# Kernel optimization log

Measured on AMD Instinct MI355X. Metric: run time of the kernel, lower is better.

The kernel has to match this reference:

```python
import jax, jax.numpy as jnp
import numpy as np

B, S, D_IN, D_OUT = 4, 2048, 1024, 1024

def setup_inputs() -> dict:
    key = jax.random.key(0)
    kx, kq, kk, kv = jax.random.split(key, 4)
    x = jax.random.normal(kx, (B, S, D_IN), dtype=jnp.float32)
    # nn.Linear weights are [d_out, d_in]; init scale ~ 1/sqrt(d_in)
    sc = 1.0 / np.sqrt(D_IN)
    Wq = jax.random.uniform(kq, (D_OUT, D_IN), minval=-sc, maxval=sc, dtype=jnp.float32)
    Wk = jax.random.uniform(kk, (D_OUT, D_IN), minval=-sc, maxval=sc, dtype=jnp.float32)
    Wv = jax.random.uniform(kv, (D_OUT, D_IN), minval=-sc, maxval=sc, dtype=jnp.float32)
    return {"x": x, "Wq": Wq, "Wk": Wk, "Wv": Wv}

def reference(x, Wq, Wk, Wv):
    # QKV projections (Linear without bias): y = x @ W.T
    q = jnp.einsum('bsd,od->bso', x, Wq)
    k = jnp.einsum('bsd,od->bso', x, Wk)
    v = jnp.einsum('bsd,od->bso', x, Wv)
    scores = jnp.einsum('bqo,bko->bqk', q, k)
    # NOTE: original code calls masked_fill non-in-place and discards the
    # result, so no causal mask is actually applied. Faithful: no mask.
    scale = 1.0 / jnp.sqrt(jnp.asarray(k.shape[-1], dtype=scores.dtype))
    weights = jax.nn.softmax(scores * scale, axis=-1)
    # dropout p=0.0 -> identity
    return jnp.einsum('bqk,bko->bqo', weights, v)
```

## Files before the change

### kernel.cpp

```cpp
#include <hip/hip_runtime.h>
#include <hip/hip_bf16.h>
#include <stdint.h>


typedef short bf16x8 __attribute__((ext_vector_type(8)));
typedef float f32x4  __attribute__((ext_vector_type(4)));
typedef unsigned short ushortx8 __attribute__((ext_vector_type(8)));

__device__ __forceinline__ unsigned short f2bf(float f) {
  unsigned u = __float_as_uint(f);
  u += 0x7fff + ((u >> 16) & 1);
  return (unsigned short)(u >> 16);
}

__global__ __launch_bounds__(256) void cvt_bf16(const float* __restrict__ src,
                                                unsigned short* __restrict__ dst) {
  int i = (blockIdx.x * 256 + threadIdx.x) * 4;
  float4 v = *(const float4*)(src + i);
  ushort4 o;
  o.x = f2bf(v.x); o.y = f2bf(v.y); o.z = f2bf(v.z); o.w = f2bf(v.w);
  *(ushort4*)(dst + i) = o;
}

__device__ __forceinline__ void gload_lds16(const void* g, void* l) {
  __builtin_amdgcn_global_load_lds(
      (const __attribute__((address_space(1))) unsigned int*)g,
      (__attribute__((address_space(3))) unsigned int*)l, 16, 0, 0);
}

template<int STORE>
__global__ __launch_bounds__(256, 2) void gemm_nt(
    const unsigned short* __restrict__ A, const unsigned short* __restrict__ B,
    void* __restrict__ Cv, int lda, int ldb, int ldc, int K,
    long strideA, long strideB, long strideC, float scale) {
  __shared__ __align__(16) unsigned short lds[2][2][128 * 32];
  const int tid  = threadIdx.x;
  const int lane = tid & 63;
  const int wid  = tid >> 6;
  const int bz   = blockIdx.z;
  const unsigned short* Ab = A + (size_t)bz * strideA;
  const unsigned short* Bb = B + (size_t)bz * strideB;
  const int row0 = blockIdx.x * 128;
  const int col0 = blockIdx.y * 128;

  f32x4 acc[4][4];
#pragma unroll
  for (int m = 0; m < 4; ++m)
#pragma unroll
    for (int n = 0; n < 4; ++n) acc[m][n] = f32x4{0.f, 0.f, 0.f, 0.f};

  const int KT = K >> 5;

  auto stage = [&](int buf, int kt) {
    const int k0 = kt << 5;
#pragma unroll
    for (int it = 0; it < 2; ++it) {
      int j   = it * 256 + tid;
      int r   = j >> 2;
      int kg  = j & 3;
      int kgS = kg ^ ((r >> 1) & 3);
      gload_lds16(Ab + (size_t)(row0 + r) * lda + k0 + kgS * 8, &lds[buf][0][j * 8]);
      gload_lds16(Bb + (size_t)(col0 + r) * ldb + k0 + kgS * 8, &lds[buf][1][j * 8]);
    }
  };

  stage(0, 0);
  int buf = 0;
  for (int kt = 0; kt < KT; ++kt) {
    __syncthreads();
    if (kt + 1 < KT) stage(buf ^ 1, kt + 1);
    const unsigned short* As = &lds[buf][0][0];
    const unsigned short* Bs = &lds[buf][1][0];
    const int kg = lane >> 4;
    const int lr = lane & 15;
    bf16x8 af[4], bfr[4];
#pragma unroll
    for (int m = 0; m < 4; ++m) {
      int r = ((wid >> 1) * 64) + m * 16 + lr;
      af[m] = *(const bf16x8*)(As + r * 32 + ((kg ^ ((r >> 1) & 3)) * 8));
    }
#pragma unroll
    for (int n = 0; n < 4; ++n) {
      int c = ((wid & 1) * 64) + n * 16 + lr;
      bfr[n] = *(const bf16x8*)(Bs + c * 32 + ((kg ^ ((c >> 1) & 3)) * 8));
    }
#pragma unroll
    for (int m = 0; m < 4; ++m)
#pragma unroll
      for (int n = 0; n < 4; ++n)
        acc[m][n] = __builtin_amdgcn_mfma_f32_16x16x32_bf16(af[m], bfr[n], acc[m][n], 0, 0, 0);
    buf ^= 1;
  }

  const int wr0 = row0 + (wid >> 1) * 64;
  const int wc0 = col0 + (wid & 1) * 64;
  const int rj  = lane >> 4;
  const int cl  = lane & 15;
#pragma unroll
  for (int m = 0; m < 4; ++m) {
#pragma unroll
    for (int n = 0; n < 4; ++n) {
#pragma unroll
      for (int j = 0; j < 4; ++j) {
        int r = wr0 + m * 16 + rj * 4 + j;
        int c = wc0 + n * 16 + cl;
        float val = acc[m][n][j];
        if constexpr (STORE == 0) {
          unsigned short* C = (unsigned short*)Cv + (size_t)bz * strideC;
          C[(size_t)r * ldc + c] = f2bf(val);
        } else if constexpr (STORE == 1) {
          float* C = (float*)Cv + (size_t)bz * strideC;
          C[(size_t)r * ldc + c] = val * scale;
        } else {
          unsigned short* C = (unsigned short*)Cv;
          size_t idx = ((size_t)(r >> 11) * 1024 + c) * 2048 + (size_t)(r & 2047);
          C[idx] = f2bf(val);
        }
      }
    }
  }
}

__global__ __launch_bounds__(256) void softmax_rows(const float* __restrict__ S,
                                                    unsigned short* __restrict__ P) {
  const size_t row = blockIdx.x;
  const float* s = S + row * 2048;
  unsigned short* p = P + row * 2048;
  const int tid  = threadIdx.x;
  const int lane = tid & 63;
  const int wid  = tid >> 6;
  float4 a = *(const float4*)(s + tid * 8);
  float4 b = *(const float4*)(s + tid * 8 + 4);
  float v[8] = {a.x, a.y, a.z, a.w, b.x, b.y, b.z, b.w};
  float mx = v[0];
#pragma unroll
  for (int i = 1; i < 8; ++i) mx = fmaxf(mx, v[i]);
#pragma unroll
  for (int o = 1; o < 64; o <<= 1) mx = fmaxf(mx, __shfl_xor(mx, o));
  __shared__ float redm[4], reds[4];
  if (lane == 0) redm[wid] = mx;
  __syncthreads();
  mx = fmaxf(fmaxf(redm[0], redm[1]), fmaxf(redm[2], redm[3]));
  float sum = 0.f;
#pragma unroll
  for (int i = 0; i < 8; ++i) { v[i] = __expf(v[i] - mx); sum += v[i]; }
#pragma unroll
  for (int o = 1; o < 64; o <<= 1) sum += __shfl_xor(sum, o);
  if (lane == 0) reds[wid] = sum;
  __syncthreads();
  sum = (reds[0] + reds[1]) + (reds[2] + reds[3]);
  float inv = 1.f / sum;
  ushortx8 o8;
#pragma unroll
  for (int i = 0; i < 8; ++i) o8[i] = f2bf(v[i] * inv);
  *(ushortx8*)(p + tid * 8) = o8;
}

extern "C" void kernel_launch(void* const* d_in, const int* in_sizes, int n_in,
                              void* d_out, int out_size, void* d_ws, size_t ws_size,
                              hipStream_t stream) {
  const float* x  = (const float*)d_in[0];
  const float* Wq = (const float*)d_in[1];
  const float* Wk = (const float*)d_in[2];
  const float* Wv = (const float*)d_in[3];

  char* w = (char*)d_ws;
  unsigned short* xb  = (unsigned short*)(w);
  unsigned short* wqk = (unsigned short*)(w + (16ull << 20));
  unsigned short* wv  = (unsigned short*)(w + (20ull << 20));
  unsigned short* QK  = (unsigned short*)(w + (22ull << 20));
  unsigned short* Vt  = (unsigned short*)(w + (54ull << 20));
  unsigned short* P   = (unsigned short*)(w + (70ull << 20));
  float*          Sc  = (float*)        (w + (102ull << 20));

  cvt_bf16<<<8192, 256, 0, stream>>>(x,  xb);
  cvt_bf16<<<1024, 256, 0, stream>>>(Wq, wqk);
  cvt_bf16<<<1024, 256, 0, stream>>>(Wk, wqk + (1u << 20));
  cvt_bf16<<<1024, 256, 0, stream>>>(Wv, wv);

  gemm_nt<0><<<dim3(64, 8, 2), 256, 0, stream>>>(
      xb, wqk, QK, 1024, 1024, 1024, 1024, 0, 1ll << 20, 8ll << 20, 1.f);
  gemm_nt<2><<<dim3(64, 8, 1), 256, 0, stream>>>(
      xb, wv, Vt, 1024, 1024, 0, 1024, 0, 0, 0, 1.f);
  gemm_nt<1><<<dim3(16, 16, 4), 256, 0, stream>>>(
      QK, QK + (8u << 20), Sc, 1024, 1024, 2048, 1024,
      2ll << 20, 2ll << 20, 4ll << 20, 0.03125f);
  softmax_rows<<<8192, 256, 0, stream>>>(Sc, P);
  gemm_nt<1><<<dim3(16, 8, 4), 256, 0, stream>>>(
      P, Vt, d_out, 2048, 2048, 1024, 2048,
      4ll << 20, 2ll << 20, 2ll << 20, 1.f);
}
```

Baseline: 271.2 us.

## Rewrite attention pipeline with 256x256 8-wave GEMM and fused unnormalized softmax

Replaces the 128x128 GEMM with a 512-thread, 256x256-tile GEMM using a 64KB double-buffered LDS schedule, interleaved loads, barriers and raised MFMA priority. The three projections are fused into one launch over a concatenated weight matrix. Softmax is folded into the QK^T epilogue: exp without max subtraction, with row sums accumulated by atomics, and normalization applied in the PV epilogue. This removes the fp32 score write and read and the separate softmax pass. It risks overflow when scores are large, since no max is subtracted, and depends on atomic ordering for the row sums.

Result: slower. 282.2 us (+4.1%).

```diff
diff --git a/kernel.cpp b/kernel.cpp
--- a/kernel.cpp
+++ b/kernel.cpp
@@ -5,7 +5,6 @@
 
 typedef short bf16x8 __attribute__((ext_vector_type(8)));
 typedef float f32x4  __attribute__((ext_vector_type(4)));
-typedef unsigned short ushortx8 __attribute__((ext_vector_type(8)));
 
 __device__ __forceinline__ unsigned short f2bf(float f) {
   unsigned u = __float_as_uint(f);
@@ -22,138 +21,197 @@
   *(ushort4*)(dst + i) = o;
 }
 
-__device__ __forceinline__ void gload_lds16(const void* g, void* l) {
+__global__ __launch_bounds__(256) void cvt_w3(const float* __restrict__ q,
+                                              const float* __restrict__ k,
+                                              const float* __restrict__ v,
+                                              unsigned short* __restrict__ dst) {
+  int b = blockIdx.x;
+  const float* s = (b < 1024) ? q : (b < 2048) ? k : v;
+  int off = (b & 1023) * 1024 + threadIdx.x * 4;
+  float4 x = *(const float4*)(s + off);
+  ushort4 o;
+  o.x = f2bf(x.x); o.y = f2bf(x.y); o.z = f2bf(x.z); o.w = f2bf(x.w);
+  *(ushort4*)(dst + b * 1024 + threadIdx.x * 4) = o;
+}
+
+__global__ __launch_bounds__(256) void invert8k(float* __restrict__ p) {
+  int i = blockIdx.x * 256 + threadIdx.x;
+  p[i] = 1.0f / p[i];
+}
+
+__device__ __forceinline__ void gl16(const unsigned short* g, char* l) {
   __builtin_amdgcn_global_load_lds(
       (const __attribute__((address_space(1))) unsigned int*)g,
       (__attribute__((address_space(3))) unsigned int*)l, 16, 0, 0);
 }
 
+#define BAR() __builtin_amdgcn_s_barrier()
+#define VMC(n) asm volatile("s_waitcnt vmcnt(" #n ")" ::: "memory")
+
 template<int STORE>
-__global__ __launch_bounds__(256, 2) void gemm_nt(
+__global__ __launch_bounds__(512, 2) void gemm8(
     const unsigned short* __restrict__ A, const unsigned short* __restrict__ B,
-    void* __restrict__ Cv, int lda, int ldb, int ldc, int K,
-    long strideA, long strideB, long strideC, float scale) {
-  __shared__ __align__(16) unsigned short lds[2][2][128 * 32];
-  const int tid  = threadIdx.x;
-  const int lane = tid & 63;
-  const int wid  = tid >> 6;
-  const int bz   = blockIdx.z;
-  const unsigned short* Ab = A + (size_t)bz * strideA;
-  const unsigned short* Bb = B + (size_t)bz * strideB;
-  const int row0 = blockIdx.x * 128;
-  const int col0 = blockIdx.y * 128;
-
-  f32x4 acc[4][4];
-#pragma unroll
-  for (int m = 0; m < 4; ++m)
-#pragma unroll
-    for (int n = 0; n < 4; ++n) acc[m][n] = f32x4{0.f, 0.f, 0.f, 0.f};
-
-  const int KT = K >> 5;
-
-  auto stage = [&](int buf, int kt) {
-    const int k0 = kt << 5;
-#pragma unroll
-    for (int it = 0; it < 2; ++it) {
-      int j   = it * 256 + tid;
-      int r   = j >> 2;
-      int kg  = j & 3;
-      int kgS = kg ^ ((r >> 1) & 3);
-      gload_lds16(Ab + (size_t)(row0 + r) * lda + k0 + kgS * 8, &lds[buf][0][j * 8]);
-      gload_lds16(Bb + (size_t)(col0 + r) * ldb + k0 + kgS * 8, &lds[buf][1][j * 8]);
-    }
-  };
-
-  stage(0, 0);
-  int buf = 0;
-  for (int kt = 0; kt < KT; ++kt) {
-    __syncthreads();
-    if (kt + 1 < KT) stage(buf ^ 1, kt + 1);
-    const unsigned short* As = &lds[buf][0][0];
-    const unsigned short* Bs = &lds[buf][1][0];
-    const int kg = lane >> 4;
-    const int lr = lane & 15;
-    bf16x8 af[4], bfr[4];
-#pragma unroll
-    for (int m = 0; m < 4; ++m) {
-      int r = ((wid >> 1) * 64) + m * 16 + lr;
-      af[m] = *(const bf16x8*)(As + r * 32 + ((kg ^ ((r >> 1) & 3)) * 8));
-    }
-#pragma unroll
-    for (int n = 0; n < 4; ++n) {
-      int c = ((wid & 1) * 64) + n * 16 + lr;
-      bfr[n] = *(const bf16x8*)(Bs + c * 32 + ((kg ^ ((c >> 1) & 3)) * 8));
-    }
-#pragma unroll
-    for (int m = 0; m < 4; ++m)
-#pragma unroll
-      for (int n = 0; n < 4; ++n)
-        acc[m][n] = __builtin_amdgcn_mfma_f32_16x16x32_bf16(af[m], bfr[n], acc[m][n], 0, 0, 0);
-    buf ^= 1;
+    long sA, long sB, int lda, int ldb, int K,
+    void* __restrict__ o0, void* __restrict__ o1) {
+  __shared__ __align__(16) char smem[131072];
+  const int tid = threadIdx.x, lane = tid & 63, wid = tid >> 6;
+  const int wm = wid >> 2, wn = wid & 3;
+  const int bz = blockIdx.z;
+  const unsigned short* Ab = A + (size_t)bz * sA;
+  const unsigned short* Bb = B + (size_t)bz * sB;
+  const int row0 = blockIdx.x << 8, col0 = blockIdx.y << 8;
+
+  const int sgr = wid * 8 + (lane >> 3);
+  const int sgk = ((lane & 7) ^ (lane >> 3)) * 8;
+  const int sgl = (wid * 64 + lane) * 16;
+  const unsigned short* pS[4];
+  pS[0] = Ab + (size_t)(row0 + sgr) * lda + sgk;
+  pS[1] = Bb + (size_t)(col0 + sgr) * ldb + sgk;
+  pS[2] = pS[0] + (size_t)128 * lda;
+  pS[3] = pS[1] + (size_t)128 * ldb;
+  const int hOff[4] = {0, 32768, 16384, 49152};
+
+  auto STG = [&](int h, int t) {
+    char* d = smem + ((t & 1) << 16) + hOff[h] + sgl;
+    const unsigned short* s = pS[h] + t * 64;
+    int ld = (h & 1) ? ldb : lda;
+    gl16(s, d);
+    gl16(s + (size_t)64 * ld, d + 8192);
+  };
+
+  bf16x8 aF[4][2], bF[2][2];
+  const int aBase = (wm * 64 + (lane & 15)) * 128;
+  const int bBase = (wn * 32 + (lane & 15)) * 128;
+  const int k0off = (((lane >> 4) ^ (lane & 7))) * 16;
+  const int k1off = (((4 + (lane >> 4)) ^ (lane & 7))) * 16;
+  auto RDA = [&](int slot, int mh) {
+#pragma unroll
+    for (int im = 0; im < 4; ++im) {
+      const char* p = smem + (slot << 16) + mh * 16384 + aBase + im * 2048;
+      aF[im][0] = *(const bf16x8*)(p + k0off);
+      aF[im][1] = *(const bf16x8*)(p + k1off);
+    }
+  };
+  auto RDB = [&](int slot, int nh) {
+#pragma unroll
+    for (int in = 0; in < 2; ++in) {
+      const char* p = smem + (slot << 16) + 32768 + nh * 16384 + bBase + in * 2048;
+      bF[in][0] = *(const bf16x8*)(p + k0off);
+      bF[in][1] = *(const bf16x8*)(p + k1off);
+    }
+  };
+
+  f32x4 acc[8][4];
+#pragma unroll
+  for (int im = 0; im < 8; ++im)
+#pragma unroll
+    for (int in = 0; in < 4; ++in) acc[im][in] = f32x4{0.f, 0.f, 0.f, 0.f};
+
+  auto MM = [&](int mh, int nh) {
+    __builtin_amdgcn_s_setprio(1);
+#pragma unroll
+    for (int im = 0; im < 4; ++im)
+#pragma unroll
+      for (int in = 0; in < 2; ++in) {
+        f32x4& c = acc[mh * 4 + im][nh * 2 + in];
+        c = __builtin_amdgcn_mfma_f32_16x16x32_bf16(aF[im][0], bF[in][0], c, 0, 0, 0);
+        c = __builtin_amdgcn_mfma_f32_16x16x32_bf16(aF[im][1], bF[in][1], c, 0, 0, 0);
+      }
+    __builtin_amdgcn_s_setprio(0);
+  };
+
+  STG(0, 0); STG(1, 0); STG(2, 0); STG(3, 0);
+  STG(1, 1); STG(2, 1); STG(3, 1);
+  VMC(6);
+  BAR();
+
+  const int NI = K >> 7;
+  for (int i = 0; i < NI - 1; ++i) {
+    const int t1 = 2 * i + 1, t2 = 2 * i + 2, t3 = 2 * i + 3;
+    RDA(0, 0); RDB(0, 0); STG(0, t1); BAR(); MM(0, 0); BAR();
+    RDA(0, 1);            STG(1, t2); BAR(); MM(1, 0); BAR();
+    RDB(0, 1);            STG(2, t2); BAR(); MM(1, 1); BAR();
+    RDA(0, 0);            STG(3, t2); VMC(6); BAR(); MM(0, 1); BAR();
+    RDA(1, 0); RDB(1, 0); STG(0, t2); BAR(); MM(0, 0); BAR();
+    RDA(1, 1);            STG(1, t3); BAR(); MM(1, 0); BAR();
+    RDB(1, 1);            STG(2, t3); BAR(); MM(1, 1); BAR();
+    RDA(1, 0);            STG(3, t3); VMC(6); BAR(); MM(0, 1); BAR();
   }
-
-  const int wr0 = row0 + (wid >> 1) * 64;
-  const int wc0 = col0 + (wid & 1) * 64;
-  const int rj  = lane >> 4;
-  const int cl  = lane & 15;
-#pragma unroll
-  for (int m = 0; m < 4; ++m) {
-#pragma unroll
-    for (int n = 0; n < 4; ++n) {
+  {
+    const int t1 = 2 * NI - 1;
+    RDA(0, 0); RDB(0, 0); STG(0, t1); BAR(); MM(0, 0); BAR();
+    RDA(0, 1); BAR(); MM(1, 0); BAR();
+    RDB(0, 1); BAR(); MM(1, 1); BAR();
+    RDA(0, 0); VMC(0); BAR(); MM(0, 1); BAR();
+    RDA(1, 0); RDB(1, 0); BAR(); MM(0, 0); BAR();
+    RDA(1, 1); BAR(); MM(1, 0); BAR();
+    RDB(1, 1); BAR(); MM(1, 1); BAR();
+    RDA(1, 0); BAR(); MM(0, 1);
+  }
+
+  const int rj = (lane >> 4) * 4;
+  const int cl = lane & 15;
+  if constexpr (STORE == 0) {
+    unsigned short* QK = (unsigned short*)o0;
+    unsigned short* Vt = (unsigned short*)o1;
+#pragma unroll
+    for (int im = 0; im < 8; ++im) {
+      int rg = row0 + wm * 64 + (im & 3) * 16 + (im >> 2) * 128 + rj;
+#pragma unroll
+      for (int in = 0; in < 4; ++in) {
+        int cg = col0 + wn * 32 + (in & 1) * 16 + (in >> 1) * 128 + cl;
+#pragma unroll
+        for (int j = 0; j < 4; ++j) {
+          int r = rg + j;
+          unsigned short bv = f2bf(acc[im][in][j]);
+          if (cg < 2048) {
+            QK[(size_t)(cg >> 10) * 8388608 + (size_t)r * 1024 + (cg & 1023)] = bv;
+          } else {
+            Vt[(size_t)(r >> 11) * 2097152 + (size_t)(cg - 2048) * 2048 + (r & 2047)] = bv;
+          }
+        }
+      }
+    }
+  } else if constexpr (STORE == 1) {
+    unsigned short* E = (unsigned short*)o0 + (size_t)bz * 4194304;
+    float* rs = (float*)o1 + bz * 2048;
+    const float SC = 0.04508422003f;
+#pragma unroll
+    for (int im = 0; im < 8; ++im) {
+      int rg = row0 + wm * 64 + (im & 3) * 16 + (im >> 2) * 128 + rj;
 #pragma unroll
       for (int j = 0; j < 4; ++j) {
-        int r = wr0 + m * 16 + rj * 4 + j;
-        int c = wc0 + n * 16 + cl;
-        float val = acc[m][n][j];
-        if constexpr (STORE == 0) {
-          unsigned short* C = (unsigned short*)Cv + (size_t)bz * strideC;
-          C[(size_t)r * ldc + c] = f2bf(val);
-        } else if constexpr (STORE == 1) {
-          float* C = (float*)Cv + (size_t)bz * strideC;
-          C[(size_t)r * ldc + c] = val * scale;
-        } else {
-          unsigned short* C = (unsigned short*)Cv;
-          size_t idx = ((size_t)(r >> 11) * 1024 + c) * 2048 + (size_t)(r & 2047);
-          C[idx] = f2bf(val);
+        int r = rg + j;
+        float part = 0.f;
+#pragma unroll
+        for (int in = 0; in < 4; ++in) {
+          int cg = col0 + wn * 32 + (in & 1) * 16 + (in >> 1) * 128 + cl;
+          unsigned short eb = f2bf(exp2f(acc[im][in][j] * SC));
+          E[(size_t)r * 2048 + cg] = eb;
+          part += __uint_as_float((unsigned)eb << 16);
         }
+#pragma unroll
+        for (int o = 1; o < 16; o <<= 1) part += __shfl_xor(part, o);
+        if (cl == 0) atomicAdd(&rs[r], part);
+      }
+    }
+  } else {
+    float* O = (float*)o0 + (size_t)bz * 2097152;
+    const float* ri = (const float*)o1 + bz * 2048;
+#pragma unroll
+    for (int im = 0; im < 8; ++im) {
+      int rg = row0 + wm * 64 + (im & 3) * 16 + (im >> 2) * 128 + rj;
+#pragma unroll
+      for (int j = 0; j < 4; ++j) {
+        float inv = ri[rg + j];
+#pragma unroll
+        for (int in = 0; in < 4; ++in) {
+          int cg = col0 + wn * 32 + (in & 1) * 16 + (in >> 1) * 128 + cl;
+          O[(size_t)(rg + j) * 1024 + cg] = acc[im][in][j] * inv;
+        }
       }
     }
   }
-}
-
-__global__ __launch_bounds__(256) void softmax_rows(const float* __restrict__ S,
-                                                    unsigned short* __restrict__ P) {
-  const size_t row = blockIdx.x;
-  const float* s = S + row * 2048;
-  unsigned short* p = P + row * 2048;
-  const int tid  = threadIdx.x;
-  const int lane = tid & 63;
-  const int wid  = tid >> 6;
-  float4 a = *(const float4*)(s + tid * 8);
-  float4 b = *(const float4*)(s + tid * 8 + 4);
-  float v[8] = {a.x, a.y, a.z, a.w, b.x, b.y, b.z, b.w};
-  float mx = v[0];
-#pragma unroll
-  for (int i = 1; i < 8; ++i) mx = fmaxf(mx, v[i]);
-#pragma unroll
-  for (int o = 1; o < 64; o <<= 1) mx = fmaxf(mx, __shfl_xor(mx, o));
-  __shared__ float redm[4], reds[4];
-  if (lane == 0) redm[wid] = mx;
-  __syncthreads();
-  mx = fmaxf(fmaxf(redm[0], redm[1]), fmaxf(redm[2], redm[3]));
-  float sum = 0.f;
-#pragma unroll
-  for (int i = 0; i < 8; ++i) { v[i] = __expf(v[i] - mx); sum += v[i]; }
-#pragma unroll
-  for (int o = 1; o < 64; o <<= 1) sum += __shfl_xor(sum, o);
-  if (lane == 0) reds[wid] = sum;
-  __syncthreads();
-  sum = (reds[0] + reds[1]) + (reds[2] + reds[3]);
-  float inv = 1.f / sum;
-  ushortx8 o8;
-#pragma unroll
-  for (int i = 0; i < 8; ++i) o8[i] = f2bf(v[i] * inv);
-  *(ushortx8*)(p + tid * 8) = o8;
 }
 
 extern "C" void kernel_launch(void* const* d_in, const int* in_sizes, int n_in,
@@ -165,28 +223,22 @@
   const float* Wv = (const float*)d_in[3];
 
   char* w = (char*)d_ws;
-  unsigned short* xb  = (unsigned short*)(w);
-  unsigned short* wqk = (unsigned short*)(w + (16ull << 20));
-  unsigned short* wv  = (unsigned short*)(w + (20ull << 20));
-  unsigned short* QK  = (unsigned short*)(w + (22ull << 20));
-  unsigned short* Vt  = (unsigned short*)(w + (54ull << 20));
-  unsigned short* P   = (unsigned short*)(w + (70ull << 20));
-  float*          Sc  = (float*)        (w + (102ull << 20));
-
-  cvt_bf16<<<8192, 256, 0, stream>>>(x,  xb);
-  cvt_bf16<<<1024, 256, 0, stream>>>(Wq, wqk);
-  cvt_bf16<<<1024, 256, 0, stream>>>(Wk, wqk + (1u << 20));
-  cvt_bf16<<<1024, 256, 0, stream>>>(Wv, wv);
-
-  gemm_nt<0><<<dim3(64, 8, 2), 256, 0, stream>>>(
-      xb, wqk, QK, 1024, 1024, 1024, 1024, 0, 1ll << 20, 8ll << 20, 1.f);
-  gemm_nt<2><<<dim3(64, 8, 1), 256, 0, stream>>>(
-      xb, wv, Vt, 1024, 1024, 0, 1024, 0, 0, 0, 1.f);
-  gemm_nt<1><<<dim3(16, 16, 4), 256, 0, stream>>>(
-      QK, QK + (8u << 20), Sc, 1024, 1024, 2048, 1024,
-      2ll << 20, 2ll << 20, 4ll << 20, 0.03125f);
-  softmax_rows<<<8192, 256, 0, stream>>>(Sc, P);
-  gemm_nt<1><<<dim3(16, 8, 4), 256, 0, stream>>>(
-      P, Vt, d_out, 2048, 2048, 1024, 2048,
-      4ll << 20, 2ll << 20, 2ll << 20, 1.f);
-}
+  unsigned short* xb = (unsigned short*)(w);
+  unsigned short* W3 = (unsigned short*)(w + (16ull << 20));
+  unsigned short* QK = (unsigned short*)(w + (22ull << 20));
+  unsigned short* Vt = (unsigned short*)(w + (54ull << 20));
+  unsigned short* E  = (unsigned short*)(w + (70ull << 20));
+  float*          rs = (float*)        (w + (102ull << 20));
+
+  hipMemsetAsync(rs, 0, 8192 * sizeof(float), stream);
+  cvt_bf16<<<8192, 256, 0, stream>>>(x, xb);
+  cvt_w3<<<3072, 256, 0, stream>>>(Wq, Wk, Wv, W3);
+
+  gemm8<0><<<dim3(32, 12, 1), 512, 0, stream>>>(
+      xb, W3, 0, 0, 1024, 1024, 1024, QK, Vt);
+  gemm8<1><<<dim3(8, 8, 4), 512, 0, stream>>>(
+      QK, QK + 8388608, 2097152, 2097152, 1024, 1024, 1024, E, rs);
+  invert8k<<<32, 256, 0, stream>>>(rs);
+  gemm8<2><<<dim3(8, 4, 4), 512, 0, stream>>>(
+      E, Vt, 4194304, 2097152, 2048, 2048, 2048, d_out, rs);
+}
```
